# Performance work log

Measured on AMD Instinct MI355X. Metric: run time of the kernel, lower is better.

The kernel has to match this reference:

```python
import jax, jax.numpy as jnp
import numpy as np

N_HEADS = 16
K_CH = 1024 // N_HEADS  # 64
SCALE = 1.0 / np.sqrt(K_CH)


def setup_inputs() -> dict:
    key = jax.random.key(0)
    ks = jax.random.split(key, 10)
    B, C, T = 4, 1024, 2048
    Cout = 1024
    xavier = lambda k, o, i: jax.random.uniform(k, (o, i), jnp.float32, -1.0, 1.0) * np.sqrt(6.0 / (o + i))
    return {
        "x": jax.random.normal(ks[0], (B, C, T), jnp.float32),
        "c": jax.random.normal(ks[1], (B, C, T), jnp.float32),
        "Wq": xavier(ks[2], C, C), "bq": jnp.zeros((C,), jnp.float32),
        "Wk": xavier(ks[3], C, C), "bk": jnp.zeros((C,), jnp.float32),
        "Wv": xavier(ks[4], C, C), "bv": jnp.zeros((C,), jnp.float32),
        "Wo": xavier(ks[5], Cout, C), "bo": jnp.zeros((Cout,), jnp.float32),
    }


def reference(x, c, Wq, bq, Wk, bk, Wv, bv, Wo, bo):
    B, C, T = x.shape
    H, K = N_HEADS, K_CH
    # 1x1 Conv1d == per-timestep linear: [O,C] @ [B,C,T] -> [B,O,T]
    q = jnp.einsum('oc,bct->bot', Wq, x) + bq[None, :, None]
    k = jnp.einsum('oc,bct->bot', Wk, c) + bk[None, :, None]
    v = jnp.einsum('oc,bct->bot', Wv, c) + bv[None, :, None]
    # split heads: b (h k) t -> b h k t
    q = q.reshape(B, H, K, T)
    k = k.reshape(B, H, K, -1)
    v = v.reshape(B, H, K, -1)
    scores = jnp.einsum('bhkt,bhks->bhts', q, k) * SCALE  # [B,H,Tt,Ts]
    p = jax.nn.softmax(scores, axis=-1)
    out = jnp.einsum('bhts,bhks->bhkt', p, v)  # b h k t
    out = out.reshape(B, H * K, T)
    return jnp.einsum('oc,bct->bot', Wo, out) + bo[None, :, None]
```

## Files before the change

### kernel.cpp

```cpp
#include <hip/hip_runtime.h>
#include <stdint.h>

typedef __bf16 bf16x8 __attribute__((ext_vector_type(8)));
typedef float f32x4 __attribute__((ext_vector_type(4)));
typedef float f32x16 __attribute__((ext_vector_type(16)));
typedef unsigned u32x2 __attribute__((ext_vector_type(2)));
typedef unsigned u32x4 __attribute__((ext_vector_type(4)));

#define LOG2E 1.44269504088896340736f
#define ATT_SCALE 0.125f
#define CL (ATT_SCALE * LOG2E)
#define SWZ(row, colb) ((colb) ^ (((row) & 7) << 4))

#define GLOAD_LDS16(gp, lp)                                                  \
  __builtin_amdgcn_global_load_lds(                                          \
      (const __attribute__((address_space(1))) void*)(gp),                   \
      (__attribute__((address_space(3))) void*)(lp), 16, 0, 0)

__device__ __forceinline__ unsigned short f2bf(float f) {
  unsigned int x = __float_as_uint(f);
  x += 0x7fffu + ((x >> 16) & 1u);
  return (unsigned short)(x >> 16);
}

__device__ __forceinline__ float fexp2(float x) {
#if __has_builtin(__builtin_amdgcn_exp2f)
  return __builtin_amdgcn_exp2f(x);
#else
  return exp2f(x);
#endif
}

__device__ __forceinline__ unsigned cvtpk(float lo, float hi) {
  unsigned r;
  asm("v_cvt_pk_bf16_f32 %0, %1, %2" : "=v"(r) : "v"(lo), "v"(hi));
  return r;
}

__device__ __forceinline__ u32x2 plswap(unsigned a, unsigned b) {
#if __has_builtin(__builtin_amdgcn_permlane32_swap)
  return __builtin_amdgcn_permlane32_swap(a, b, false, false);
#else
  unsigned ax = (unsigned)__shfl_xor((int)a, 32);
  unsigned bx = (unsigned)__shfl_xor((int)b, 32);
  int hi = (threadIdx.x & 32) ? 1 : 0;
  u32x2 r;
  r[0] = hi ? bx : a;
  r[1] = hi ? b : ax;
  return r;
#endif
}

__global__ __launch_bounds__(256) void cvt_weights(
    const float* __restrict__ w0, const float* __restrict__ w1,
    const float* __restrict__ w2, const float* __restrict__ w3,
    unsigned short* __restrict__ o0, unsigned short* __restrict__ o1,
    unsigned short* __restrict__ o2, unsigned short* __restrict__ o3) {
  int sel = blockIdx.x >> 10;
  const float* in = sel == 0 ? w0 : sel == 1 ? w1 : sel == 2 ? w2 : w3;
  unsigned short* out = sel == 0 ? o0 : sel == 1 ? o1 : sel == 2 ? o2 : o3;
  float scale = sel == 0 ? CL : 1.0f;
  int i = ((blockIdx.x & 1023) * 256 + threadIdx.x) * 4;
  float4 v = *(const float4*)(in + i);
  ushort4 o;
  o.x = f2bf(v.x * scale); o.y = f2bf(v.y * scale);
  o.z = f2bf(v.z * scale); o.w = f2bf(v.w * scale);
  *(ushort4*)(out + i) = o;
}

__global__ __launch_bounds__(256) void transpose_cvt2(const float* __restrict__ x,
                                                      const float* __restrict__ c,
                                                      unsigned short* __restrict__ xT,
                                                      unsigned short* __restrict__ cT) {
  __shared__ unsigned short tile[32][33];
  const int C = 1024, T = 2048;
  int z = blockIdx.z;
  const float* in = (z < 4) ? x : c;
  unsigned short* out = (z < 4) ? xT : cT;
  int b = z & 3;
  int t0 = blockIdx.x * 32, c0 = blockIdx.y * 32;
  int tx = threadIdx.x & 31, ty = threadIdx.x >> 5;
  const float* src = in + ((size_t)b * C + c0) * T + t0;
  #pragma unroll
  for (int i = 0; i < 4; ++i) {
    int cc = ty + i * 8;
    tile[cc][tx] = f2bf(src[(size_t)cc * T + tx]);
  }
  __syncthreads();
  unsigned short* dst = out + ((size_t)b * T + t0) * C + c0;
  #pragma unroll
  for (int i = 0; i < 4; ++i) {
    int tt = ty + i * 8;
    dst[(size_t)tt * C + tx] = tile[tx][tt];
  }
}

template <int NT, int OUT_F32>
__device__ __forceinline__ void gemm_core128(
    const unsigned short* __restrict__ A, const unsigned short* __restrict__ B,
    void* __restrict__ Cv, const float* __restrict__ bias, int bias_is_m,
    float bs, int m0, int n0, int ldC) {
  __shared__ __align__(16) char lds[3 * 16384];
  const int tid = threadIdx.x;
  const int l = tid & 63, w = tid >> 6;
  const int g = l >> 4, j = l & 15;
  const int wr = w >> 1, wc = w & 1;

  const int r0 = tid >> 3;
  const int slotp = (tid & 7) ^ (r0 & 7);
  const int mloc = r0 * 2 + (slotp >> 2);
  const int kg = slotp & 3;
  const unsigned short* ga0 = A + (size_t)(m0 + mloc) * 1024 + kg * 8;
  const unsigned short* ga1 = A + (size_t)(m0 + 64 + mloc) * 1024 + kg * 8;
  const unsigned short* gb0 = B + (size_t)(n0 + mloc) * 1024 + kg * 8;
  const unsigned short* gb1 = B + (size_t)(n0 + 64 + mloc) * 1024 + kg * 8;

  auto stage = [&](char* buf) {
    GLOAD_LDS16(ga0, buf + tid * 16);
    GLOAD_LDS16(ga1, buf + 4096 + tid * 16);
    GLOAD_LDS16(gb0, buf + 8192 + tid * 16);
    GLOAD_LDS16(gb1, buf + 12288 + tid * 16);
    ga0 += 32; ga1 += 32; gb0 += 32; gb1 += 32;
  };

  f32x4 acc[4][4] = {};

  stage(lds);
  stage(lds + 16384);

  char* bufc = lds;
  char* bufs = lds + 2 * 16384;

  for (int t = 0; t < NT; ++t) {
    if (t == NT - 1) asm volatile("s_waitcnt vmcnt(0)" ::: "memory");
    else             asm volatile("s_waitcnt vmcnt(4)" ::: "memory");
    __builtin_amdgcn_s_barrier();
    asm volatile("" ::: "memory");
    if (t < NT - 2) stage(bufs);

    bf16x8 af[4], bfr[4];
    #pragma unroll
    for (int mf = 0; mf < 4; ++mf) {
      int m = wr * 64 + mf * 16 + j;
      int rp = m >> 1;
      int cb = ((m & 1) * 64 + g * 16) ^ ((rp & 7) << 4);
      af[mf] = *(const bf16x8*)(bufc + rp * 128 + cb);
    }
    #pragma unroll
    for (int nf = 0; nf < 4; ++nf) {
      int n = wc * 64 + nf * 16 + j;
      int rp = n >> 1;
      int cb = ((n & 1) * 64 + g * 16) ^ ((rp & 7) << 4);
      bfr[nf] = *(const bf16x8*)(bufc + 8192 + rp * 128 + cb);
    }
    #pragma unroll
    for (int mf = 0; mf < 4; ++mf)
      #pragma unroll
      for (int nf = 0; nf < 4; ++nf)
        acc[mf][nf] = __builtin_amdgcn_mfma_f32_16x16x32_bf16(af[mf], bfr[nf], acc[mf][nf], 0, 0, 0);

    bufc += 16384; if (bufc == lds + 49152) bufc = lds;
    bufs += 16384; if (bufs == lds + 49152) bufs = lds;
  }

  #pragma unroll
  for (int mf = 0; mf < 4; ++mf) {
    #pragma unroll
    for (int rr = 0; rr < 4; ++rr) {
      int m = m0 + wr * 64 + mf * 16 + g * 4 + rr;
      float bm = bias_is_m ? bias[m] * bs : 0.f;
      #pragma unroll
      for (int nf = 0; nf < 4; ++nf) {
        int n = n0 + wc * 64 + nf * 16 + j;
        float val = acc[mf][nf][rr] + bm + (bias_is_m ? 0.f : bias[n] * bs);
        if (OUT_F32) ((float*)Cv)[(size_t)m * ldC + n] = val;
        else ((unsigned short*)Cv)[(size_t)m * ldC + n] = f2bf(val);
      }
    }
  }
}

__global__ __launch_bounds__(256, 3) void qkv_gemm3(
    const unsigned short* __restrict__ xT, const unsigned short* __restrict__ cT,
    const unsigned short* __restrict__ wq, const unsigned short* __restrict__ wk,
    const unsigned short* __restrict__ wv,
    const float* __restrict__ bq, const float* __restrict__ bk,
    const float* __restrict__ bv,
    unsigned short* __restrict__ QT, unsigned short* __restrict__ KT,
    unsigned short* __restrict__ Vb) {
  const size_t sBT = (size_t)2048 * 1024;
  const int id = (blockIdx.x & 7) * 192 + (blockIdx.x >> 3);
  const int op = id >> 9;
  const int r = id & 511;
  const int z = r >> 7;
  const unsigned short *A, *B;
  unsigned short* Cp;
  const float* bias;
  int m0, n0, ldC, bias_is_m;
  float bs;
  if (op == 2) {
    n0 = (r & 15) * 128; m0 = ((r >> 4) & 7) * 128;
    A = wv; B = cT + z * sBT; Cp = Vb + z * (size_t)1024 * 2048;
    bias = bv; ldC = 2048; bias_is_m = 1; bs = 1.0f;
  } else {
    n0 = (r & 7) * 128; m0 = ((r >> 3) & 15) * 128;
    A = (op == 0 ? xT : cT) + z * sBT;
    B = (op == 0 ? wq : wk);
    Cp = (op == 0 ? QT : KT) + z * sBT;
    bias = (op == 0 ? bq : bk); ldC = 1024; bias_is_m = 0;
    bs = (op == 0) ? CL : 1.0f;
  }
  gemm_core128<32, 0>(A, B, Cp, bias, bias_is_m, bs, m0, n0, ldC);
}

__global__ __launch_bounds__(256, 3) void gemm_out3(
    const unsigned short* __restrict__ Wo, const unsigned short* __restrict__ OT,
    float* __restrict__ Out, const float* __restrict__ bias) {
  const size_t sBT = (size_t)2048 * 1024;
  const int id = (blockIdx.x & 7) * 64 + (blockIdx.x >> 3);
  const int z = id >> 7;
  const int m0 = ((id >> 4) & 7) * 128, n0 = (id & 15) * 128;
  gemm_core128<32, 1>(Wo, OT + z * sBT, Out + z * (size_t)1024 * 2048,
                      bias, 1, 1.0f, m0, n0, 2048);
}

__global__ __launch_bounds__(256, 3) void attn_kernel4(const unsigned short* __restrict__ QT,
                                                       const unsigned short* __restrict__ KT,
                                                       const unsigned short* __restrict__ V,
                                                       unsigned short* __restrict__ OT) {
  __shared__ __align__(16) char kv[2][16384];
  __shared__ float lbuf[4][32];

  const int fid = blockIdx.x;
  const int xcd = fid & 7, idx = fid >> 3;
  const int bh = ((idx & 7) << 3) | xcd;
  const int tblk = idx >> 3;
  const int b = bh >> 4, h = bh & 15;

  const int tid = threadIdx.x;
  const int w = tid >> 6, l = tid & 63, lo5 = l & 31, hi = l >> 5;
  const int tq0 = tblk * 128 + w * 32;

  bf16x8 q[4];
  {
    const unsigned short* Qb = QT + ((size_t)(b * 2048 + tq0 + lo5)) * 1024 + h * 64 + hi * 8;
    #pragma unroll
    for (int kb = 0; kb < 4; ++kb) q[kb] = *(const bf16x8*)(Qb + kb * 16);
  }

  f32x16 o[2] = {};
  float lr = 0.f;

  const int srow0 = tid >> 3, sslot = tid & 7;
  const unsigned short* Kg0 = KT + ((size_t)b * 2048) * 1024 + h * 64;
  const unsigned short* Vg0 = V + ((size_t)(b * 1024 + h * 64)) * 2048;

  auto stage = [&](int bsel, int s0) {
    char* Ks = kv[bsel];
    char* Vs = kv[bsel] + 8192;
    #pragma unroll
    for (int p = 0; p < 2; ++p) {
      int row = p * 32 + srow0;
      int ch = sslot ^ (row & 7);
      GLOAD_LDS16(Kg0 + (size_t)(s0 + row) * 1024 + ch * 8, Ks + (p * 256 + tid) * 16);
      GLOAD_LDS16(Vg0 + (size_t)row * 2048 + s0 + ch * 8, Vs + (p * 256 + tid) * 16);
    }
  };

  stage(0, 0);
  __syncthreads();

  for (int t = 0; t < 32; ++t) {
    int cur = t & 1;
    if (t < 31) stage(cur ^ 1, (t + 1) * 64);
    char* Ks = kv[cur];
    char* Vs = kv[cur] + 8192;

    f32x16 p0 = {}, p1 = {};
    #pragma unroll
    for (int kb = 0; kb < 4; ++kb) {
      int r0 = lo5, r1 = 32 + lo5;
      bf16x8 ka0 = *(const bf16x8*)(Ks + r0 * 128 + SWZ(r0, kb * 32 + hi * 16));
      bf16x8 ka1 = *(const bf16x8*)(Ks + r1 * 128 + SWZ(r1, kb * 32 + hi * 16));
      p0 = __builtin_amdgcn_mfma_f32_32x32x16_bf16(ka0, q[kb], p0, 0, 0, 0);
      p1 = __builtin_amdgcn_mfma_f32_32x32x16_bf16(ka1, q[kb], p1, 0, 0, 0);
    }

    float ls0 = 0.f, ls1 = 0.f, ls2 = 0.f, ls3 = 0.f;
    #pragma unroll
    for (int r = 0; r < 16; r += 4) {
      float e0 = fexp2(p0[r]), e1 = fexp2(p0[r + 1]), e2 = fexp2(p0[r + 2]), e3 = fexp2(p0[r + 3]);
      p0[r] = e0; p0[r + 1] = e1; p0[r + 2] = e2; p0[r + 3] = e3;
      ls0 += e0; ls1 += e1; ls2 += e2; ls3 += e3;
    }
    #pragma unroll
    for (int r = 0; r < 16; r += 4) {
      float e0 = fexp2(p1[r]), e1 = fexp2(p1[r + 1]), e2 = fexp2(p1[r + 2]), e3 = fexp2(p1[r + 3]);
      p1[r] = e0; p1[r + 1] = e1; p1[r + 2] = e2; p1[r + 3] = e3;
      ls0 += e0; ls1 += e1; ls2 += e2; ls3 += e3;
    }
    lr += (ls0 + ls1) + (ls2 + ls3);

    u32x4 pa[4];
    {
      u32x2 ra = plswap(cvtpk(p0[0], p0[1]), cvtpk(p0[4], p0[5]));
      u32x2 rb = plswap(cvtpk(p0[2], p0[3]), cvtpk(p0[6], p0[7]));
      pa[0] = (u32x4){ra[0], rb[0], ra[1], rb[1]};
      u32x2 rc = plswap(cvtpk(p0[8], p0[9]), cvtpk(p0[12], p0[13]));
      u32x2 rd = plswap(cvtpk(p0[10], p0[11]), cvtpk(p0[14], p0[15]));
      pa[1] = (u32x4){rc[0], rd[0], rc[1], rd[1]};
      u32x2 re = plswap(cvtpk(p1[0], p1[1]), cvtpk(p1[4], p1[5]));
      u32x2 rf = plswap(cvtpk(p1[2], p1[3]), cvtpk(p1[6], p1[7]));
      pa[2] = (u32x4){re[0], rf[0], re[1], rf[1]};
      u32x2 rg = plswap(cvtpk(p1[8], p1[9]), cvtpk(p1[12], p1[13]));
      u32x2 rh = plswap(cvtpk(p1[10], p1[11]), cvtpk(p1[14], p1[15]));
      pa[3] = (u32x4){rg[0], rh[0], rg[1], rh[1]};
    }

    #pragma unroll
    for (int sb = 0; sb < 4; ++sb)
      #pragma unroll
      for (int kb2 = 0; kb2 < 2; ++kb2) {
        int row = kb2 * 32 + lo5;
        bf16x8 vb = *(const bf16x8*)(Vs + row * 128 + SWZ(row, sb * 32 + hi * 16));
        o[kb2] = __builtin_amdgcn_mfma_f32_32x32x16_bf16(
            __builtin_bit_cast(bf16x8, pa[sb]), vb, o[kb2], 0, 0, 0);
      }
    __syncthreads();
  }

  u32x2 sw = plswap(__float_as_uint(lr), __float_as_uint(lr));
  float lt = __uint_as_float(sw[0]) + __uint_as_float(sw[1]);
  if (hi == 0) lbuf[w][lo5] = 1.0f / lt;
  unsigned short* Ob = OT + ((size_t)(b * 2048 + tq0)) * 1024 + h * 64 + lo5;
  #pragma unroll
  for (int r = 0; r < 16; ++r) {
    int srow = (r & 3) + 8 * (r >> 2) + 4 * hi;
    float inv = lbuf[w][srow];
    Ob[(size_t)srow * 1024 + 0]  = f2bf(o[0][r] * inv);
    Ob[(size_t)srow * 1024 + 32] = f2bf(o[1][r] * inv);
  }
}

extern "C" void kernel_launch(void* const* d_in, const int* in_sizes, int n_in,
                              void* d_out, int out_size, void* d_ws, size_t ws_size,
                              hipStream_t stream) {
  const float* x  = (const float*)d_in[0];
  const float* c  = (const float*)d_in[1];
  const float* Wq = (const float*)d_in[2];
  const float* bq = (const float*)d_in[3];
  const float* Wk = (const float*)d_in[4];
  const float* bk = (const float*)d_in[5];
  const float* Wv = (const float*)d_in[6];
  const float* bv = (const float*)d_in[7];
  const float* Wo = (const float*)d_in[8];
  const float* bo = (const float*)d_in[9];

  const size_t MB = 1024 * 1024;
  char* ws = (char*)d_ws;
  unsigned short* wqb = (unsigned short*)(ws + 0 * MB);
  unsigned short* wkb = (unsigned short*)(ws + 2 * MB);
  unsigned short* wvb = (unsigned short*)(ws + 4 * MB);
  unsigned short* wob = (unsigned short*)(ws + 6 * MB);
  unsigned short* xT  = (unsigned short*)(ws + 8 * MB);
  unsigned short* cT  = (unsigned short*)(ws + 24 * MB);
  unsigned short* QT  = (unsigned short*)(ws + 40 * MB);
  unsigned short* KT  = (unsigned short*)(ws + 56 * MB);
  unsigned short* Vb  = (unsigned short*)(ws + 72 * MB);
  unsigned short* OT  = xT;

  cvt_weights<<<dim3(4096), 256, 0, stream>>>(Wq, Wk, Wv, Wo, wqb, wkb, wvb, wob);
  transpose_cvt2<<<dim3(64, 32, 8), 256, 0, stream>>>(x, c, xT, cT);

  qkv_gemm3<<<dim3(1536), 256, 0, stream>>>(xT, cT, wqb, wkb, wvb, bq, bk, bv, QT, KT, Vb);

  attn_kernel4<<<dim3(1024), 256, 0, stream>>>(QT, KT, Vb, OT);

  gemm_out3<<<dim3(512), 256, 0, stream>>>(wob, OT, (float*)d_out, bo);
}
```

Baseline: 196.2 us.

## Compute softmax row sums with MFMA against ones instead of VALU adds

The attention kernel drops the per-element VALU accumulation of exponentials and instead computes the row sums with one extra MFMA per key sub-block, multiplying P by a vector of bf16 ones. This also removes the final LDS exchange and its buffer. Launch bounds go from 3 to 4 blocks per CU, and permlane32_swap is now emitted through inline asm. The sums are taken from bf16-rounded P, which matches the numerator, but the extra MFMA work and tighter register limits could cause spills.

```diff
diff --git a/kernel.cpp b/kernel.cpp
--- a/kernel.cpp
+++ b/kernel.cpp
@@ -38,17 +38,11 @@
 }
 
 __device__ __forceinline__ u32x2 plswap(unsigned a, unsigned b) {
-#if __has_builtin(__builtin_amdgcn_permlane32_swap)
-  return __builtin_amdgcn_permlane32_swap(a, b, false, false);
-#else
-  unsigned ax = (unsigned)__shfl_xor((int)a, 32);
-  unsigned bx = (unsigned)__shfl_xor((int)b, 32);
-  int hi = (threadIdx.x & 32) ? 1 : 0;
+  asm("v_permlane32_swap_b32 %0, %1" : "+v"(a), "+v"(b));
   u32x2 r;
-  r[0] = hi ? bx : a;
-  r[1] = hi ? b : ax;
+  r[0] = a;
+  r[1] = b;
   return r;
-#endif
 }
 
 __global__ __launch_bounds__(256) void cvt_weights(
@@ -224,12 +218,11 @@
                       bias, 1, 1.0f, m0, n0, 2048);
 }
 
-__global__ __launch_bounds__(256, 3) void attn_kernel4(const unsigned short* __restrict__ QT,
+__global__ __launch_bounds__(256, 4) void attn_kernel5(const unsigned short* __restrict__ QT,
                                                        const unsigned short* __restrict__ KT,
                                                        const unsigned short* __restrict__ V,
                                                        unsigned short* __restrict__ OT) {
   __shared__ __align__(16) char kv[2][16384];
-  __shared__ float lbuf[4][32];
 
   const int fid = blockIdx.x;
   const int xcd = fid & 7, idx = fid >> 3;
@@ -249,7 +242,10 @@
   }
 
   f32x16 o[2] = {};
-  float lr = 0.f;
+  f32x16 ol = {};
+
+  const unsigned one2 = 0x3F803F80u;
+  const bf16x8 ones = __builtin_bit_cast(bf16x8, (u32x4){one2, one2, one2, one2});
 
   const int srow0 = tid >> 3, sslot = tid & 7;
   const unsigned short* Kg0 = KT + ((size_t)b * 2048) * 1024 + h * 64;
@@ -286,20 +282,10 @@
       p1 = __builtin_amdgcn_mfma_f32_32x32x16_bf16(ka1, q[kb], p1, 0, 0, 0);
     }
 
-    float ls0 = 0.f, ls1 = 0.f, ls2 = 0.f, ls3 = 0.f;
-    #pragma unroll
-    for (int r = 0; r < 16; r += 4) {
-      float e0 = fexp2(p0[r]), e1 = fexp2(p0[r + 1]), e2 = fexp2(p0[r + 2]), e3 = fexp2(p0[r + 3]);
-      p0[r] = e0; p0[r + 1] = e1; p0[r + 2] = e2; p0[r + 3] = e3;
-      ls0 += e0; ls1 += e1; ls2 += e2; ls3 += e3;
-    }
-    #pragma unroll
-    for (int r = 0; r < 16; r += 4) {
-      float e0 = fexp2(p1[r]), e1 = fexp2(p1[r + 1]), e2 = fexp2(p1[r + 2]), e3 = fexp2(p1[r + 3]);
-      p1[r] = e0; p1[r + 1] = e1; p1[r + 2] = e2; p1[r + 3] = e3;
-      ls0 += e0; ls1 += e1; ls2 += e2; ls3 += e3;
-    }
-    lr += (ls0 + ls1) + (ls2 + ls3);
+    #pragma unroll
+    for (int r = 0; r < 16; ++r) p0[r] = fexp2(p0[r]);
+    #pragma unroll
+    for (int r = 0; r < 16; ++r) p1[r] = fexp2(p1[r]);
 
     u32x4 pa[4];
     {
@@ -318,25 +304,24 @@
     }
 
     #pragma unroll
-    for (int sb = 0; sb < 4; ++sb)
+    for (int sb = 0; sb < 4; ++sb) {
+      bf16x8 pab = __builtin_bit_cast(bf16x8, pa[sb]);
       #pragma unroll
       for (int kb2 = 0; kb2 < 2; ++kb2) {
         int row = kb2 * 32 + lo5;
         bf16x8 vb = *(const bf16x8*)(Vs + row * 128 + SWZ(row, sb * 32 + hi * 16));
-        o[kb2] = __builtin_amdgcn_mfma_f32_32x32x16_bf16(
-            __builtin_bit_cast(bf16x8, pa[sb]), vb, o[kb2], 0, 0, 0);
+        o[kb2] = __builtin_amdgcn_mfma_f32_32x32x16_bf16(pab, vb, o[kb2], 0, 0, 0);
       }
+      ol = __builtin_amdgcn_mfma_f32_32x32x16_bf16(pab, ones, ol, 0, 0, 0);
+    }
     __syncthreads();
   }
 
-  u32x2 sw = plswap(__float_as_uint(lr), __float_as_uint(lr));
-  float lt = __uint_as_float(sw[0]) + __uint_as_float(sw[1]);
-  if (hi == 0) lbuf[w][lo5] = 1.0f / lt;
   unsigned short* Ob = OT + ((size_t)(b * 2048 + tq0)) * 1024 + h * 64 + lo5;
   #pragma unroll
   for (int r = 0; r < 16; ++r) {
     int srow = (r & 3) + 8 * (r >> 2) + 4 * hi;
-    float inv = lbuf[w][srow];
+    float inv = 1.0f / ol[r];
     Ob[(size_t)srow * 1024 + 0]  = f2bf(o[0][r] * inv);
     Ob[(size_t)srow * 1024 + 32] = f2bf(o[1][r] * inv);
   }
@@ -374,7 +359,7 @@
 
   qkv_gemm3<<<dim3(1536), 256, 0, stream>>>(xT, cT, wqb, wkb, wvb, bq, bk, bv, QT, KT, Vb);
 
-  attn_kernel4<<<dim3(1024), 256, 0, stream>>>(QT, KT, Vb, OT);
+  attn_kernel5<<<dim3(1024), 256, 0, stream>>>(QT, KT, Vb, OT);
 
   gemm_out3<<<dim3(512), 256, 0, stream>>>(wob, OT, (float*)d_out, bo);
 }
```

After: 189.6 us. 1.03x faster.
